# Kernel tuning notes

Hardware: AMD Instinct MI355X
Metric: run time of the kernel (lower is better)

The kernel has to match this reference:

```python
import jax, jax.numpy as jnp
import numpy as np

O_DIM, A_DIM, Z_DIM = 256, 8, 9
D, H, L, M, B = 128, 128, 4, 4, 65536  # module dim, MLP hidden, n_layers, n_modules, batch


def setup_inputs() -> dict:
    key = jax.random.key(0)
    ks = jax.random.split(key, 18)
    s = 0.05
    return {
        "o": jax.random.normal(ks[0], (B, O_DIM), jnp.float32),
        "z_map": jax.random.uniform(ks[1], (B, Z_DIM), jnp.float32),
        "collision_prob": jax.random.uniform(ks[2], (B, 1), jnp.float32),
        # base obs embedding and routing (task) embedding
        "Wb": jax.random.normal(ks[3], (O_DIM, D), jnp.float32) * s,
        "bb": jnp.zeros((D,), jnp.float32),
        "Wz": jax.random.normal(ks[4], (Z_DIM + 1, D), jnp.float32) * s,
        "bz": jnp.zeros((D,), jnp.float32),
        # L layers x M modules of DxD linears
        "Wm": jax.random.normal(ks[5], (L, M, D, D), jnp.float32) * s,
        "bm": jnp.zeros((L, M, D), jnp.float32),
        # routing heads: L-1 inter-layer (M*M) gates + final (M,) gate
        "Wg": jax.random.normal(ks[6], (L - 1, D, M * M), jnp.float32) * s,
        "Wg_last": jax.random.normal(ks[7], (D, M), jnp.float32) * s,
        # dueling heads
        "Wv": jax.random.normal(ks[8], (D, 1), jnp.float32) * s,
        "bv": jnp.zeros((1,), jnp.float32),
        "Wa1": jax.random.normal(ks[9], (D, H), jnp.float32) * s,
        "ba1": jnp.zeros((H,), jnp.float32),
        "Wa2": jax.random.normal(ks[10], (H, A_DIM), jnp.float32) * s,
        "ba2": jnp.zeros((A_DIM,), jnp.float32),
    }


def _softmodule(o, z_map, collision_prob, Wb, bb, Wz, bz, Wm, bm, Wg, Wg_last):
    f0 = jax.nn.relu(o @ Wb + bb)                              # (B, D)
    z_in = jnp.concatenate([z_map, collision_prob], axis=-1)   # (B, Z+1)
    g = jax.nn.relu(z_in @ Wz + bz) * f0                       # routing embedding (B, D)
    # layer 0: all modules consume the obs embedding
    x = jax.nn.relu(jnp.einsum("bd,mde->bme", f0, Wm[0]) + bm[0])  # (B, M, D)
    for l in range(1, L):
        logits = (g @ Wg[l - 1]).reshape(-1, M, M)             # (B, i, j)
        p = jax.nn.softmax(logits, axis=1)                     # soft routing over incoming modules i
        xin = jnp.einsum("bij,bid->bjd", p, x)                 # weighted gather-combine
        x = jax.nn.relu(jnp.einsum("bmd,mde->bme", xin, Wm[l]) + bm[l])
    p_last = jax.nn.softmax(g @ Wg_last, axis=-1)              # (B, M)
    return jnp.einsum("bm,bmd->bd", p_last, x)                 # (B, D)


def reference(o, z_map, collision_prob, Wb, bb, Wz, bz, Wm, bm, Wg, Wg_last,
              Wv, bv, Wa1, ba1, Wa2, ba2):
    feature = _softmodule(o, z_map, collision_prob, Wb, bb, Wz, bz, Wm, bm, Wg, Wg_last)
    value = feature @ Wv + bv                                  # (B, 1)
    adv = jax.nn.relu(feature @ Wa1 + ba1) @ Wa2 + ba2         # (B, A)
    adv = adv - adv.mean(axis=-1, keepdims=True)
    return adv + value
```

## Files before the change

### kernel.cpp

```cpp
#include <hip/hip_runtime.h>
#include <stdint.h>


typedef __attribute__((ext_vector_type(8))) short short8;
typedef __attribute__((ext_vector_type(4))) float f32x4;
typedef __attribute__((ext_vector_type(2))) float f32x2;
typedef __attribute__((address_space(1))) const unsigned int u32_g;
typedef __attribute__((address_space(3))) unsigned int u32_l;

__device__ __forceinline__ unsigned short f2bf(float f) {
  union { float f; uint32_t u; } v; v.f = f;
  uint32_t r = v.u + 0x7FFFu + ((v.u >> 16) & 1u);
  return (unsigned short)(r >> 16);
}
__device__ __forceinline__ float blo(uint32_t w) { union { uint32_t u; float f; } c; c.u = w << 16; return c.f; }
__device__ __forceinline__ float bhi(uint32_t w) { union { uint32_t u; float f; } c; c.u = w & 0xffff0000u; return c.f; }
__device__ __forceinline__ uint32_t packrne(float lo, float hi) {
  union { float f; uint32_t u; } a, b; a.f = lo; b.f = hi;
  uint32_t ra = a.u + 0x7fffu + ((a.u >> 16) & 1u);
  uint32_t rb = b.u + 0x7fffu + ((b.u >> 16) & 1u);
  return (ra >> 16) | (rb & 0xffff0000u);
}
__device__ __forceinline__ f32x2 unpk2(uint32_t w) {
  f32x2 r; r.x = blo(w); r.y = bhi(w); return r;
}
union S8 { short8 s; uint32_t u[4]; };

__global__ void prep_weights(const float* __restrict__ Wb, const float* __restrict__ Wm,
                             const float* __restrict__ Wa1, const float* __restrict__ Wg,
                             const float* __restrict__ Wgl, const float* __restrict__ Wa2,
                             unsigned short* __restrict__ ws) {
  int idx = blockIdx.x * 256 + threadIdx.x;
  if (idx >= 321536) return;
  unsigned short v;
  if (idx < 32768) {
    int st = idx >> 12, n = (idx >> 5) & 127, kk = idx & 31;
    v = f2bf(Wb[(st * 32 + kk) * 128 + n]);
  } else if (idx < 294912) {
    int t = idx - 32768; int lj = t >> 14; int g = t & 16383;
    int st = g >> 12, n = (g >> 5) & 127, kk = g & 31;
    v = f2bf(Wm[lj * 16384 + (st * 32 + kk) * 128 + n]);
  } else if (idx < 311296) {
    int t = idx - 294912; int st = t >> 12, n = (t >> 5) & 127, kk = t & 31;
    v = f2bf(Wa1[(st * 32 + kk) * 128 + n]);
  } else if (idx < 319488) {
    int t = idx - 311296; int st = t >> 11, n = (t >> 5) & 63, kk = t & 31;
    int k = st * 32 + kk;
    if (n < 48)      v = f2bf(Wg[(n >> 4) * 2048 + k * 16 + (n & 15)]);
    else if (n < 52) v = f2bf(Wgl[k * 4 + (n - 48)]);
    else             v = 0;
  } else {
    int t = idx - 319488; int st = t >> 9, n = (t >> 5) & 15, kk = t & 31;
    v = (n < 8) ? f2bf(Wa2[(st * 32 + kk) * 8 + n]) : (unsigned short)0;
  }
  ws[idx] = v;
}

__device__ __forceinline__ void gld16(const void* g, void* l) {
  __builtin_amdgcn_global_load_lds((u32_g*)g, (u32_l*)l, 16, 0, 0);
}

template <int BYTES>
__device__ __forceinline__ void stageW(void* wl, const unsigned short* __restrict__ src, int tid) {
  const char* g = (const char*)src;
  char* l = (char*)wl;
  int wvoff = (tid >> 6) << 10;
  int goff = wvoff | ((tid & 63) << 4);
#pragma unroll
  for (int it = 0; it < BYTES / 4096; ++it)
    gld16(g + it * 4096 + goff, l + it * 4096 + wvoff);
}

__device__ __forceinline__ void gemm128(const short8 xin[4], const unsigned short* WL,
                                        int q, int ml, f32x4 a[8]) {
#pragma unroll
  for (int nt = 0; nt < 8; ++nt) a[nt] = (f32x4){0.f, 0.f, 0.f, 0.f};
#pragma unroll
  for (int st = 0; st < 4; ++st) {
#pragma unroll
    for (int nt = 0; nt < 8; ++nt) {
      short8 bf = *(const short8*)(WL + (st * 128 + nt * 16 + ml) * 32 + q * 8);
      a[nt] = __builtin_amdgcn_mfma_f32_16x16x32_bf16(xin[st], bf, a[nt], 0, 0, 0);
    }
  }
}

__device__ __forceinline__ void combine_layer(const short8 xo[4][4],
                                              const unsigned short* __restrict__ prow,
                                              short8 xin[4][4]) {
  float p[4][4];
#pragma unroll
  for (int j = 0; j < 4; ++j) {
    uint32_t pw0 = *(const uint32_t*)(prow + j * 4);
    uint32_t pw1 = *(const uint32_t*)(prow + j * 4 + 2);
    p[j][0] = blo(pw0); p[j][1] = bhi(pw0); p[j][2] = blo(pw1); p[j][3] = bhi(pw1);
  }
#pragma unroll
  for (int st = 0; st < 4; ++st) {
    S8 x0, x1, x2, x3;
    x0.s = xo[0][st]; x1.s = xo[1][st]; x2.s = xo[2][st]; x3.s = xo[3][st];
    S8 r0, r1, r2, r3;
#pragma unroll
    for (int w = 0; w < 4; ++w) {
      f32x2 u0 = unpk2(x0.u[w]), u1 = unpk2(x1.u[w]), u2 = unpk2(x2.u[w]), u3 = unpk2(x3.u[w]);
      f32x2 s0 = p[0][0] * u0 + p[0][1] * u1 + p[0][2] * u2 + p[0][3] * u3;
      f32x2 s1 = p[1][0] * u0 + p[1][1] * u1 + p[1][2] * u2 + p[1][3] * u3;
      f32x2 s2 = p[2][0] * u0 + p[2][1] * u1 + p[2][2] * u2 + p[2][3] * u3;
      f32x2 s3 = p[3][0] * u0 + p[3][1] * u1 + p[3][2] * u2 + p[3][3] * u3;
      r0.u[w] = packrne(s0.x, s0.y); r1.u[w] = packrne(s1.x, s1.y);
      r2.u[w] = packrne(s2.x, s2.y); r3.u[w] = packrne(s3.x, s3.y);
    }
    xin[0][st] = r0.s; xin[1][st] = r1.s; xin[2][st] = r2.s; xin[3][st] = r3.s;
  }
}

__global__ __attribute__((amdgpu_flat_work_group_size(256, 256), amdgpu_waves_per_eu(2, 2)))
void dueling_fused(
    const float* __restrict__ o, const float* __restrict__ zmap, const float* __restrict__ coll,
    const float* __restrict__ bb, const float* __restrict__ Wz, const float* __restrict__ bz,
    const float* __restrict__ bm, const float* __restrict__ Wv, const float* __restrict__ bv,
    const float* __restrict__ ba1, const float* __restrict__ ba2,
    const unsigned short* __restrict__ WbF, const unsigned short* __restrict__ WmF,
    const unsigned short* __restrict__ Wa1F, const unsigned short* __restrict__ WgF,
    const unsigned short* __restrict__ Wa2F, float* __restrict__ out)
{
  __shared__ __align__(16) unsigned char smem[57344];
  unsigned short* WL    = (unsigned short*)(smem);
  float*          WLf   = (float*)(smem);
  unsigned short* xbuf  = (unsigned short*)(smem + 32768);
  unsigned short* pall  = (unsigned short*)(smem + 50176);
  float*          zbufF = (float*)(smem + 50176);
  float*          WvF   = (float*)(smem + 50176);
  float*          plast = (float*)(smem + 56320);
  float*          vbuf  = (float*)(smem + 56320);

  const int tid = threadIdx.x;
  const int wv  = tid >> 6;
  const int lane = tid & 63;
  const int q   = lane >> 4;
  const int ml  = lane & 15;
  const int row0 = blockIdx.x * 64;
  unsigned short* xbw = xbuf + wv * 2176;

  for (int i = tid; i < 640; i += 256) {
    if (i < 576) { int r = i / 9, c = i - r * 9; zbufF[r * 12 + c] = zmap[(row0 + r) * 9 + c]; }
    else         { int r = i - 576; zbufF[r * 12 + 9] = coll[row0 + r]; }
  }

  const f32x4 z4 = {0.f, 0.f, 0.f, 0.f};

  f32x4 acc[8];
#pragma unroll
  for (int nt = 0; nt < 8; ++nt) acc[nt] = z4;
  const float* orow = o + (size_t)(row0 + wv * 16 + ml) * 256;
#pragma unroll
  for (int kh = 0; kh < 2; ++kh) {
    float4 ov[8];
#pragma unroll
    for (int st = 0; st < 4; ++st) {
      const float* src = orow + kh * 128 + st * 32 + q * 8;
      ov[st * 2]     = *(const float4*)(src);
      ov[st * 2 + 1] = *(const float4*)(src + 4);
    }
    if (kh) __syncthreads();
    stageW<32768>(WL, WbF + kh * 16384, tid);
    __syncthreads();
#pragma unroll
    for (int st = 0; st < 4; ++st) {
      S8 af;
      af.u[0] = packrne(ov[st*2].x, ov[st*2].y);     af.u[1] = packrne(ov[st*2].z, ov[st*2].w);
      af.u[2] = packrne(ov[st*2+1].x, ov[st*2+1].y); af.u[3] = packrne(ov[st*2+1].z, ov[st*2+1].w);
#pragma unroll
      for (int nt = 0; nt < 8; ++nt) {
        short8 bf = *(const short8*)(WL + (st * 128 + nt * 16 + ml) * 32 + q * 8);
        acc[nt] = __builtin_amdgcn_mfma_f32_16x16x32_bf16(af.s, bf, acc[nt], 0, 0, 0);
      }
    }
  }
#pragma unroll
  for (int nt = 0; nt < 8; ++nt) {
    float bbv = bb[nt * 16 + ml];
#pragma unroll
    for (int r2 = 0; r2 < 4; ++r2) {
      float v = fmaxf(acc[nt][r2] + bbv, 0.f);
      acc[nt][r2] = v;
      xbw[(q * 4 + r2) * 136 + nt * 16 + ml] = f2bf(v);
    }
  }
  __syncthreads();
  short8 f0f[4];
#pragma unroll
  for (int st = 0; st < 4; ++st) f0f[st] = *(const short8*)(xbw + ml * 136 + st * 32 + q * 8);
  for (int i = tid; i < 1280; i += 256) WLf[i] = Wz[i];
  __syncthreads();
#pragma unroll
  for (int nt = 0; nt < 8; ++nt) {
    int col = nt * 16 + ml;
    float bzv = bz[col];
#pragma unroll
    for (int r2 = 0; r2 < 4; ++r2) {
      int row = wv * 16 + q * 4 + r2;
      float zd = bzv;
#pragma unroll
      for (int k = 0; k < 10; ++k) zd += zbufF[row * 12 + k] * WLf[k * 128 + col];
      xbw[(q * 4 + r2) * 136 + col] = f2bf(fmaxf(zd, 0.f) * acc[nt][r2]);
    }
  }
  __syncthreads();
  short8 gf[4];
#pragma unroll
  for (int st = 0; st < 4; ++st) gf[st] = *(const short8*)(xbw + ml * 136 + st * 32 + q * 8);
  stageW<16384>(WL, WgF, tid);
  __syncthreads();
#pragma unroll
  for (int nt = 0; nt < 4; ++nt) acc[nt] = z4;
#pragma unroll
  for (int st = 0; st < 4; ++st) {
#pragma unroll
    for (int nt = 0; nt < 4; ++nt) {
      short8 bf = *(const short8*)(WL + (st * 64 + nt * 16 + ml) * 32 + q * 8);
      acc[nt] = __builtin_amdgcn_mfma_f32_16x16x32_bf16(gf[st], bf, acc[nt], 0, 0, 0);
    }
  }
#pragma unroll
  for (int li = 0; li < 3; ++li) {
#pragma unroll
    for (int r2 = 0; r2 < 4; ++r2) {
      float a = acc[li][r2];
      float m = fmaxf(a, __shfl_xor(a, 4)); m = fmaxf(m, __shfl_xor(m, 8));
      float e = __expf(a - m);
      float s = e; s += __shfl_xor(s, 4); s += __shfl_xor(s, 8);
      pall[(li * 64 + wv * 16 + q * 4 + r2) * 16 + (ml & 3) * 4 + (ml >> 2)] = f2bf(e / s);
    }
  }
#pragma unroll
  for (int r2 = 0; r2 < 4; ++r2) {
    float a = acc[3][r2];
    float m = fmaxf(a, __shfl_xor(a, 1)); m = fmaxf(m, __shfl_xor(m, 2));
    float e = __expf(a - m);
    float s = e; s += __shfl_xor(s, 1); s += __shfl_xor(s, 2);
    if (ml < 4) plast[(wv * 16 + q * 4 + r2) * 4 + ml] = e / s;
  }

  short8 xo[4][4];
  f32x4 a[8];
#pragma unroll
  for (int j = 0; j < 4; ++j) {
    if (j > 0) {
#pragma unroll
      for (int st = 0; st < 4; ++st) xo[j - 1][st] = *(const short8*)(xbw + ml * 136 + st * 32 + q * 8);
    }
    __syncthreads();
    stageW<32768>(WL, WmF + j * 16384, tid);
    __syncthreads();
    gemm128(f0f, WL, q, ml, a);
#pragma unroll
    for (int nt = 0; nt < 8; ++nt) {
      float bmv = bm[j * 128 + nt * 16 + ml];
#pragma unroll
      for (int r2 = 0; r2 < 4; ++r2)
        xbw[(q * 4 + r2) * 136 + nt * 16 + ml] = f2bf(fmaxf(a[nt][r2] + bmv, 0.f));
    }
  }

  short8 xin[4][4];
  for (int l = 1; l <= 2; ++l) {
#pragma unroll
    for (int st = 0; st < 4; ++st) xo[3][st] = *(const short8*)(xbw + ml * 136 + st * 32 + q * 8);
    combine_layer(xo, pall + ((l - 1) * 64 + wv * 16 + ml) * 16, xin);
#pragma unroll
    for (int j = 0; j < 4; ++j) {
      if (j > 0) {
#pragma unroll
        for (int st = 0; st < 4; ++st) xo[j - 1][st] = *(const short8*)(xbw + ml * 136 + st * 32 + q * 8);
      }
      __syncthreads();
      stageW<32768>(WL, WmF + (l * 4 + j) * 16384, tid);
      __syncthreads();
      gemm128(xin[j], WL, q, ml, a);
#pragma unroll
      for (int nt = 0; nt < 8; ++nt) {
        float bmv = bm[(l * 4 + j) * 128 + nt * 16 + ml];
#pragma unroll
        for (int r2 = 0; r2 < 4; ++r2)
          xbw[(q * 4 + r2) * 136 + nt * 16 + ml] = f2bf(fmaxf(a[nt][r2] + bmv, 0.f));
      }
    }
  }

  f32x4 feat[8];
  {
#pragma unroll
    for (int st = 0; st < 4; ++st) xo[3][st] = *(const short8*)(xbw + ml * 136 + st * 32 + q * 8);
    combine_layer(xo, pall + (2 * 64 + wv * 16 + ml) * 16, xin);
#pragma unroll
    for (int nt = 0; nt < 8; ++nt) feat[nt] = z4;
#pragma unroll
    for (int j = 0; j < 4; ++j) {
      __syncthreads();
      stageW<32768>(WL, WmF + (12 + j) * 16384, tid);
      __syncthreads();
      gemm128(xin[j], WL, q, ml, a);
      float pl[4];
#pragma unroll
      for (int r2 = 0; r2 < 4; ++r2) pl[r2] = plast[(wv * 16 + q * 4 + r2) * 4 + j];
#pragma unroll
      for (int nt = 0; nt < 8; ++nt) {
        float bmv = bm[(12 + j) * 128 + nt * 16 + ml];
#pragma unroll
        for (int r2 = 0; r2 < 4; ++r2)
          feat[nt][r2] += pl[r2] * fmaxf(a[nt][r2] + bmv, 0.f);
      }
    }
  }

  __syncthreads();
  if (tid < 128) WvF[tid] = Wv[tid];
  if (tid == 128) WvF[128] = bv[0];
  stageW<32768>(WL, Wa1F, tid);
#pragma unroll
  for (int nt = 0; nt < 8; ++nt)
#pragma unroll
    for (int r2 = 0; r2 < 4; ++r2)
      xbw[(q * 4 + r2) * 136 + nt * 16 + ml] = f2bf(feat[nt][r2]);
  __syncthreads();
#pragma unroll
  for (int r2 = 0; r2 < 4; ++r2) {
    float v = 0.f;
#pragma unroll
    for (int nt = 0; nt < 8; ++nt) v += feat[nt][r2] * WvF[nt * 16 + ml];
    v += __shfl_xor(v, 1); v += __shfl_xor(v, 2); v += __shfl_xor(v, 4); v += __shfl_xor(v, 8);
    if (ml == 0) vbuf[wv * 16 + q * 4 + r2] = v + WvF[128];
  }
  short8 ff[4];
#pragma unroll
  for (int st = 0; st < 4; ++st) ff[st] = *(const short8*)(xbw + ml * 136 + st * 32 + q * 8);
  gemm128(ff, WL, q, ml, a);
#pragma unroll
  for (int nt = 0; nt < 8; ++nt) {
    float b1v = ba1[nt * 16 + ml];
#pragma unroll
    for (int r2 = 0; r2 < 4; ++r2)
      xbw[(q * 4 + r2) * 136 + nt * 16 + ml] = f2bf(fmaxf(a[nt][r2] + b1v, 0.f));
  }
  __syncthreads();
  stageW<4096>(WL, Wa2F, tid);
  __syncthreads();
  short8 a1f[4];
#pragma unroll
  for (int st = 0; st < 4; ++st) a1f[st] = *(const short8*)(xbw + ml * 136 + st * 32 + q * 8);
  f32x4 av = z4;
#pragma unroll
  for (int st = 0; st < 4; ++st) {
    short8 bf = *(const short8*)(WL + (st * 16 + ml) * 32 + q * 8);
    av = __builtin_amdgcn_mfma_f32_16x16x32_bf16(a1f[st], bf, av, 0, 0, 0);
  }
  float ba2v = ba2[ml & 7];
#pragma unroll
  for (int r2 = 0; r2 < 4; ++r2) {
    float aa = av[r2] + ba2v;
    float s = aa + __shfl_xor(aa, 1); s += __shfl_xor(s, 2); s += __shfl_xor(s, 4);
    if (ml < 8)
      out[(size_t)(row0 + wv * 16 + q * 4 + r2) * 8 + ml] = aa - s * 0.125f + vbuf[wv * 16 + q * 4 + r2];
  }
}

extern "C" void kernel_launch(void* const* d_in, const int* in_sizes, int n_in,
                              void* d_out, int out_size, void* d_ws, size_t ws_size,
                              hipStream_t stream) {
  const float* o   = (const float*)d_in[0];
  const float* zm  = (const float*)d_in[1];
  const float* cp  = (const float*)d_in[2];
  const float* Wb  = (const float*)d_in[3];
  const float* bb  = (const float*)d_in[4];
  const float* Wz  = (const float*)d_in[5];
  const float* bz  = (const float*)d_in[6];
  const float* Wm  = (const float*)d_in[7];
  const float* bm  = (const float*)d_in[8];
  const float* Wg  = (const float*)d_in[9];
  const float* Wgl = (const float*)d_in[10];
  const float* Wv  = (const float*)d_in[11];
  const float* bv  = (const float*)d_in[12];
  const float* Wa1 = (const float*)d_in[13];
  const float* ba1 = (const float*)d_in[14];
  const float* Wa2 = (const float*)d_in[15];
  const float* ba2 = (const float*)d_in[16];
  unsigned short* wsT = (unsigned short*)d_ws;

  int B = in_sizes[0] / 256;

  hipLaunchKernelGGL(prep_weights, dim3(1256), dim3(256), 0, stream,
                     Wb, Wm, Wa1, Wg, Wgl, Wa2, wsT);
  hipLaunchKernelGGL(dueling_fused, dim3(B / 64), dim3(256), 0, stream,
                     o, zm, cp, bb, Wz, bz, bm, Wv, bv, ba1, ba2,
                     wsT, wsT + 32768, wsT + 294912, wsT + 311296, wsT + 319488,
                     (float*)d_out);
}
```

Baseline: 251.9 us.

## Stream all weights through a triple-buffered LDS ring with async prefetch

```diff
diff --git a/kernel.cpp b/kernel.cpp
--- a/kernel.cpp
+++ b/kernel.cpp
@@ -15,6 +15,7 @@
 }
 __device__ __forceinline__ float blo(uint32_t w) { union { uint32_t u; float f; } c; c.u = w << 16; return c.f; }
 __device__ __forceinline__ float bhi(uint32_t w) { union { uint32_t u; float f; } c; c.u = w & 0xffff0000u; return c.f; }
+__device__ __forceinline__ float b2f(unsigned short h) { union { uint32_t u; float f; } c; c.u = ((uint32_t)h) << 16; return c.f; }
 __device__ __forceinline__ uint32_t packrne(float lo, float hi) {
   union { float f; uint32_t u; } a, b; a.f = lo; b.f = hi;
   uint32_t ra = a.u + 0x7fffu + ((a.u >> 16) & 1u);
@@ -36,19 +37,19 @@
   if (idx < 32768) {
     int st = idx >> 12, n = (idx >> 5) & 127, kk = idx & 31;
     v = f2bf(Wb[(st * 32 + kk) * 128 + n]);
-  } else if (idx < 294912) {
-    int t = idx - 32768; int lj = t >> 14; int g = t & 16383;
-    int st = g >> 12, n = (g >> 5) & 127, kk = g & 31;
-    v = f2bf(Wm[lj * 16384 + (st * 32 + kk) * 128 + n]);
-  } else if (idx < 311296) {
-    int t = idx - 294912; int st = t >> 12, n = (t >> 5) & 127, kk = t & 31;
-    v = f2bf(Wa1[(st * 32 + kk) * 128 + n]);
-  } else if (idx < 319488) {
-    int t = idx - 311296; int st = t >> 11, n = (t >> 5) & 63, kk = t & 31;
+  } else if (idx < 40960) {
+    int t = idx - 32768; int st = t >> 11, n = (t >> 5) & 63, kk = t & 31;
     int k = st * 32 + kk;
     if (n < 48)      v = f2bf(Wg[(n >> 4) * 2048 + k * 16 + (n & 15)]);
     else if (n < 52) v = f2bf(Wgl[k * 4 + (n - 48)]);
     else             v = 0;
+  } else if (idx < 303104) {
+    int t = idx - 40960; int lj = t >> 14; int g = t & 16383;
+    int st = g >> 12, n = (g >> 5) & 127, kk = g & 31;
+    v = f2bf(Wm[lj * 16384 + (st * 32 + kk) * 128 + n]);
+  } else if (idx < 319488) {
+    int t = idx - 303104; int st = t >> 12, n = (t >> 5) & 127, kk = t & 31;
+    v = f2bf(Wa1[(st * 32 + kk) * 128 + n]);
   } else {
     int t = idx - 319488; int st = t >> 9, n = (t >> 5) & 15, kk = t & 31;
     v = (n < 8) ? f2bf(Wa2[(st * 32 + kk) * 8 + n]) : (unsigned short)0;
@@ -60,28 +61,12 @@
   __builtin_amdgcn_global_load_lds((u32_g*)g, (u32_l*)l, 16, 0, 0);
 }
 
-template <int BYTES>
-__device__ __forceinline__ void stageW(void* wl, const unsigned short* __restrict__ src, int tid) {
-  const char* g = (const char*)src;
-  char* l = (char*)wl;
-  int wvoff = (tid >> 6) << 10;
-  int goff = wvoff | ((tid & 63) << 4);
-#pragma unroll
-  for (int it = 0; it < BYTES / 4096; ++it)
-    gld16(g + it * 4096 + goff, l + it * 4096 + wvoff);
-}
-
-__device__ __forceinline__ void gemm128(const short8 xin[4], const unsigned short* WL,
-                                        int q, int ml, f32x4 a[8]) {
-#pragma unroll
-  for (int nt = 0; nt < 8; ++nt) a[nt] = (f32x4){0.f, 0.f, 0.f, 0.f};
-#pragma unroll
-  for (int st = 0; st < 4; ++st) {
-#pragma unroll
-    for (int nt = 0; nt < 8; ++nt) {
-      short8 bf = *(const short8*)(WL + (st * 128 + nt * 16 + ml) * 32 + q * 8);
-      a[nt] = __builtin_amdgcn_mfma_f32_16x16x32_bf16(xin[st], bf, a[nt], 0, 0, 0);
-    }
+__device__ __forceinline__ void gemm32(const short8 xst, const unsigned short* C,
+                                       int q, int ml, f32x4 a[8]) {
+#pragma unroll
+  for (int nt = 0; nt < 8; ++nt) {
+    short8 bf = *(const short8*)(C + (nt * 16 + ml) * 32 + q * 8);
+    a[nt] = __builtin_amdgcn_mfma_f32_16x16x32_bf16(xst, bf, a[nt], 0, 0, 0);
   }
 }
 
@@ -114,25 +99,26 @@
   }
 }
 
-__global__ __attribute__((amdgpu_flat_work_group_size(256, 256), amdgpu_waves_per_eu(2, 2)))
+#define RSYNC2() asm volatile("s_waitcnt vmcnt(2) lgkmcnt(0)\n\ts_barrier" ::: "memory")
+#define RSYNC0() asm volatile("s_waitcnt vmcnt(0) lgkmcnt(0)\n\ts_barrier" ::: "memory")
+#define RSTEP2(PTR) do { RSYNC2(); ring_issue(); (PTR) = ring_next(); } while (0)
+#define RSTEP0(PTR) do { RSYNC0(); ring_issue(); (PTR) = ring_next(); } while (0)
+
+__global__ __attribute__((amdgpu_flat_work_group_size(256, 256), amdgpu_waves_per_eu(3)))
 void dueling_fused(
     const float* __restrict__ o, const float* __restrict__ zmap, const float* __restrict__ coll,
     const float* __restrict__ bb, const float* __restrict__ Wz, const float* __restrict__ bz,
     const float* __restrict__ bm, const float* __restrict__ Wv, const float* __restrict__ bv,
     const float* __restrict__ ba1, const float* __restrict__ ba2,
-    const unsigned short* __restrict__ WbF, const unsigned short* __restrict__ WmF,
-    const unsigned short* __restrict__ Wa1F, const unsigned short* __restrict__ WgF,
-    const unsigned short* __restrict__ Wa2F, float* __restrict__ out)
+    const unsigned short* __restrict__ ws, float* __restrict__ out)
 {
-  __shared__ __align__(16) unsigned char smem[57344];
-  unsigned short* WL    = (unsigned short*)(smem);
-  float*          WLf   = (float*)(smem);
-  unsigned short* xbuf  = (unsigned short*)(smem + 32768);
-  unsigned short* pall  = (unsigned short*)(smem + 50176);
-  float*          zbufF = (float*)(smem + 50176);
-  float*          WvF   = (float*)(smem + 50176);
-  float*          plast = (float*)(smem + 56320);
-  float*          vbuf  = (float*)(smem + 56320);
+  __shared__ __align__(16) unsigned char smem[53248];
+  unsigned short* xbuf  = (unsigned short*)(smem + 24576);
+  unsigned short* pall  = (unsigned short*)(smem + 41984);
+  float*          zbufF = (float*)(smem + 41984);
+  float*          plast = (float*)(smem + 48128);
+  float*          vbuf  = (float*)(smem + 48128);
+  unsigned short* bmL   = (unsigned short*)(smem + 49152);
 
   const int tid = threadIdx.x;
   const int wv  = tid >> 6;
@@ -146,37 +132,51 @@
     if (i < 576) { int r = i / 9, c = i - r * 9; zbufF[r * 12 + c] = zmap[(row0 + r) * 9 + c]; }
     else         { int r = i - 576; zbufF[r * 12 + 9] = coll[row0 + r]; }
   }
+  for (int i = tid; i < 2048; i += 256) bmL[i] = f2bf(bm[i]);
+
+  short8 of[8];
+  const float* orow = o + (size_t)(row0 + wv * 16 + ml) * 256;
+#pragma unroll
+  for (int st = 0; st < 8; ++st) {
+    float4 v0 = *(const float4*)(orow + st * 32 + q * 8);
+    float4 v1 = *(const float4*)(orow + st * 32 + q * 8 + 4);
+    S8 af;
+    af.u[0] = packrne(v0.x, v0.y); af.u[1] = packrne(v0.z, v0.w);
+    af.u[2] = packrne(v1.x, v1.y); af.u[3] = packrne(v1.z, v1.w);
+    of[st] = af.s;
+  }
+  asm volatile("s_waitcnt vmcnt(0) lgkmcnt(0)" ::: "memory");
+
+  int r_kiss = 0, r_riss = 0, r_rc = 0;
+  const char* r_gsrc = (const char*)ws;
+  const int wvoff = wv << 10;
+  const int goff  = wvoff | ((tid & 63) << 4);
+  auto ring_issue = [&]() {
+    if (r_kiss <= 78) {
+      char* l = (char*)smem + r_riss;
+      int srco = (r_kiss == 78) ? 0 : 4096;
+      gld16(r_gsrc + goff, l + wvoff);
+      gld16(r_gsrc + srco + goff, l + 4096 + wvoff);
+      r_gsrc += 8192;
+    }
+    ++r_kiss;
+    r_riss += 8192; if (r_riss == 24576) r_riss = 0;
+  };
+  auto ring_next = [&]() -> const unsigned short* {
+    const unsigned short* p = (const unsigned short*)(smem + r_rc);
+    r_rc += 8192; if (r_rc == 24576) r_rc = 0;
+    return p;
+  };
+  ring_issue(); ring_issue();
 
   const f32x4 z4 = {0.f, 0.f, 0.f, 0.f};
+  const unsigned short* C;
 
   f32x4 acc[8];
 #pragma unroll
   for (int nt = 0; nt < 8; ++nt) acc[nt] = z4;
-  const float* orow = o + (size_t)(row0 + wv * 16 + ml) * 256;
-#pragma unroll
-  for (int kh = 0; kh < 2; ++kh) {
-    float4 ov[8];
-#pragma unroll
-    for (int st = 0; st < 4; ++st) {
-      const float* src = orow + kh * 128 + st * 32 + q * 8;
-      ov[st * 2]     = *(const float4*)(src);
-      ov[st * 2 + 1] = *(const float4*)(src + 4);
-    }
-    if (kh) __syncthreads();
-    stageW<32768>(WL, WbF + kh * 16384, tid);
-    __syncthreads();
-#pragma unroll
-    for (int st = 0; st < 4; ++st) {
-      S8 af;
-      af.u[0] = packrne(ov[st*2].x, ov[st*2].y);     af.u[1] = packrne(ov[st*2].z, ov[st*2].w);
-      af.u[2] = packrne(ov[st*2+1].x, ov[st*2+1].y); af.u[3] = packrne(ov[st*2+1].z, ov[st*2+1].w);
-#pragma unroll
-      for (int nt = 0; nt < 8; ++nt) {
-        short8 bf = *(const short8*)(WL + (st * 128 + nt * 16 + ml) * 32 + q * 8);
-        acc[nt] = __builtin_amdgcn_mfma_f32_16x16x32_bf16(af.s, bf, acc[nt], 0, 0, 0);
-      }
-    }
-  }
+#pragma unroll
+  for (int st = 0; st < 8; ++st) { RSTEP2(C); gemm32(of[st], C, q, ml, acc); }
 #pragma unroll
   for (int nt = 0; nt < 8; ++nt) {
     float bbv = bb[nt * 16 + ml];
@@ -187,41 +187,48 @@
       xbw[(q * 4 + r2) * 136 + nt * 16 + ml] = f2bf(v);
     }
   }
-  __syncthreads();
   short8 f0f[4];
 #pragma unroll
   for (int st = 0; st < 4; ++st) f0f[st] = *(const short8*)(xbw + ml * 136 + st * 32 + q * 8);
-  for (int i = tid; i < 1280; i += 256) WLf[i] = Wz[i];
-  __syncthreads();
+
 #pragma unroll
   for (int nt = 0; nt < 8; ++nt) {
     int col = nt * 16 + ml;
+    float wz[10];
+#pragma unroll
+    for (int k = 0; k < 10; ++k) wz[k] = Wz[k * 128 + col];
     float bzv = bz[col];
 #pragma unroll
     for (int r2 = 0; r2 < 4; ++r2) {
       int row = wv * 16 + q * 4 + r2;
       float zd = bzv;
 #pragma unroll
-      for (int k = 0; k < 10; ++k) zd += zbufF[row * 12 + k] * WLf[k * 128 + col];
+      for (int k = 0; k < 10; ++k) zd += zbufF[row * 12 + k] * wz[k];
       xbw[(q * 4 + r2) * 136 + col] = f2bf(fmaxf(zd, 0.f) * acc[nt][r2]);
     }
   }
-  __syncthreads();
   short8 gf[4];
 #pragma unroll
   for (int st = 0; st < 4; ++st) gf[st] = *(const short8*)(xbw + ml * 136 + st * 32 + q * 8);
-  stageW<16384>(WL, WgF, tid);
-  __syncthreads();
+
 #pragma unroll
   for (int nt = 0; nt < 4; ++nt) acc[nt] = z4;
-#pragma unroll
-  for (int st = 0; st < 4; ++st) {
+  RSTEP0(C);
+#pragma unroll
+  for (int sp = 0; sp < 2; ++sp)
 #pragma unroll
     for (int nt = 0; nt < 4; ++nt) {
-      short8 bf = *(const short8*)(WL + (st * 64 + nt * 16 + ml) * 32 + q * 8);
-      acc[nt] = __builtin_amdgcn_mfma_f32_16x16x32_bf16(gf[st], bf, acc[nt], 0, 0, 0);
-    }
-  }
+      short8 bf = *(const short8*)(C + (sp * 64 + nt * 16 + ml) * 32 + q * 8);
+      acc[nt] = __builtin_amdgcn_mfma_f32_16x16x32_bf16(gf[sp], bf, acc[nt], 0, 0, 0);
+    }
+  RSTEP2(C);
+#pragma unroll
+  for (int sp = 0; sp < 2; ++sp)
+#pragma unroll
+    for (int nt = 0; nt < 4; ++nt) {
+      short8 bf = *(const short8*)(C + (sp * 64 + nt * 16 + ml) * 32 + q * 8);
+      acc[nt] = __builtin_amdgcn_mfma_f32_16x16x32_bf16(gf[2 + sp], bf, acc[nt], 0, 0, 0);
+    }
 #pragma unroll
   for (int li = 0; li < 3; ++li) {
 #pragma unroll
@@ -250,13 +257,13 @@
 #pragma unroll
       for (int st = 0; st < 4; ++st) xo[j - 1][st] = *(const short8*)(xbw + ml * 136 + st * 32 + q * 8);
     }
-    __syncthreads();
-    stageW<32768>(WL, WmF + j * 16384, tid);
-    __syncthreads();
-    gemm128(f0f, WL, q, ml, a);
+#pragma unroll
+    for (int nt = 0; nt < 8; ++nt) a[nt] = z4;
+#pragma unroll
+    for (int st = 0; st < 4; ++st) { RSTEP2(C); gemm32(f0f[st], C, q, ml, a); }
 #pragma unroll
     for (int nt = 0; nt < 8; ++nt) {
-      float bmv = bm[j * 128 + nt * 16 + ml];
+      float bmv = b2f(bmL[j * 128 + nt * 16 + ml]);
 #pragma unroll
       for (int r2 = 0; r2 < 4; ++r2)
         xbw[(q * 4 + r2) * 136 + nt * 16 + ml] = f2bf(fmaxf(a[nt][r2] + bmv, 0.f));
@@ -274,13 +281,13 @@
 #pragma unroll
         for (int st = 0; st < 4; ++st) xo[j - 1][st] = *(const short8*)(xbw + ml * 136 + st * 32 + q * 8);
       }
-      __syncthreads();
-      stageW<32768>(WL, WmF + (l * 4 + j) * 16384, tid);
-      __syncthreads();
-      gemm128(xin[j], WL, q, ml, a);
+#pragma unroll
+      for (int nt = 0; nt < 8; ++nt) a[nt] = z4;
+#pragma unroll
+      for (int st = 0; st < 4; ++st) { RSTEP2(C); gemm32(xin[j][st], C, q, ml, a); }
 #pragma unroll
       for (int nt = 0; nt < 8; ++nt) {
-        float bmv = bm[(l * 4 + j) * 128 + nt * 16 + ml];
+        float bmv = b2f(bmL[(l * 4 + j) * 128 + nt * 16 + ml]);
 #pragma unroll
         for (int r2 = 0; r2 < 4; ++r2)
           xbw[(q * 4 + r2) * 136 + nt * 16 + ml] = f2bf(fmaxf(a[nt][r2] + bmv, 0.f));
@@ -297,16 +304,16 @@
     for (int nt = 0; nt < 8; ++nt) feat[nt] = z4;
 #pragma unroll
     for (int j = 0; j < 4; ++j) {
-      __syncthreads();
-      stageW<32768>(WL, WmF + (12 + j) * 16384, tid);
-      __syncthreads();
-      gemm128(xin[j], WL, q, ml, a);
+#pragma unroll
+      for (int nt = 0; nt < 8; ++nt) a[nt] = z4;
+#pragma unroll
+      for (int st = 0; st < 4; ++st) { RSTEP2(C); gemm32(xin[j][st], C, q, ml, a); }
       float pl[4];
 #pragma unroll
       for (int r2 = 0; r2 < 4; ++r2) pl[r2] = plast[(wv * 16 + q * 4 + r2) * 4 + j];
 #pragma unroll
       for (int nt = 0; nt < 8; ++nt) {
-        float bmv = bm[(12 + j) * 128 + nt * 16 + ml];
+        float bmv = b2f(bmL[(12 + j) * 128 + nt * 16 + ml]);
 #pragma unroll
         for (int r2 = 0; r2 < 4; ++r2)
           feat[nt][r2] += pl[r2] * fmaxf(a[nt][r2] + bmv, 0.f);
@@ -314,28 +321,34 @@
     }
   }
 
-  __syncthreads();
-  if (tid < 128) WvF[tid] = Wv[tid];
-  if (tid == 128) WvF[128] = bv[0];
-  stageW<32768>(WL, Wa1F, tid);
 #pragma unroll
   for (int nt = 0; nt < 8; ++nt)
 #pragma unroll
     for (int r2 = 0; r2 < 4; ++r2)
       xbw[(q * 4 + r2) * 136 + nt * 16 + ml] = f2bf(feat[nt][r2]);
-  __syncthreads();
-#pragma unroll
-  for (int r2 = 0; r2 < 4; ++r2) {
-    float v = 0.f;
-#pragma unroll
-    for (int nt = 0; nt < 8; ++nt) v += feat[nt][r2] * WvF[nt * 16 + ml];
-    v += __shfl_xor(v, 1); v += __shfl_xor(v, 2); v += __shfl_xor(v, 4); v += __shfl_xor(v, 8);
-    if (ml == 0) vbuf[wv * 16 + q * 4 + r2] = v + WvF[128];
-  }
   short8 ff[4];
 #pragma unroll
   for (int st = 0; st < 4; ++st) ff[st] = *(const short8*)(xbw + ml * 136 + st * 32 + q * 8);
-  gemm128(ff, WL, q, ml, a);
+#pragma unroll
+  for (int nt = 0; nt < 8; ++nt) a[nt] = z4;
+#pragma unroll
+  for (int st = 0; st < 4; ++st) { RSTEP2(C); gemm32(ff[st], C, q, ml, a); }
+
+  {
+    float wvv[8];
+#pragma unroll
+    for (int nt = 0; nt < 8; ++nt) wvv[nt] = Wv[nt * 16 + ml];
+    float bvv = bv[0];
+#pragma unroll
+    for (int r2 = 0; r2 < 4; ++r2) {
+      float v = 0.f;
+#pragma unroll
+      for (int nt = 0; nt < 8; ++nt) v += feat[nt][r2] * wvv[nt];
+      v += __shfl_xor(v, 1); v += __shfl_xor(v, 2); v += __shfl_xor(v, 4); v += __shfl_xor(v, 8);
+      if (ml == 0) vbuf[wv * 16 + q * 4 + r2] = v + bvv;
+    }
+  }
+
 #pragma unroll
   for (int nt = 0; nt < 8; ++nt) {
     float b1v = ba1[nt * 16 + ml];
@@ -343,16 +356,15 @@
     for (int r2 = 0; r2 < 4; ++r2)
       xbw[(q * 4 + r2) * 136 + nt * 16 + ml] = f2bf(fmaxf(a[nt][r2] + b1v, 0.f));
   }
-  __syncthreads();
-  stageW<4096>(WL, Wa2F, tid);
-  __syncthreads();
   short8 a1f[4];
 #pragma unroll
   for (int st = 0; st < 4; ++st) a1f[st] = *(const short8*)(xbw + ml * 136 + st * 32 + q * 8);
+
+  RSTEP0(C);
   f32x4 av = z4;
 #pragma unroll
   for (int st = 0; st < 4; ++st) {
-    short8 bf = *(const short8*)(WL + (st * 16 + ml) * 32 + q * 8);
+    short8 bf = *(const short8*)(C + (st * 16 + ml) * 32 + q * 8);
     av = __builtin_amdgcn_mfma_f32_16x16x32_bf16(a1f[st], bf, av, 0, 0, 0);
   }
   float ba2v = ba2[ml & 7];
@@ -393,6 +405,5 @@
                      Wb, Wm, Wa1, Wg, Wgl, Wa2, wsT);
   hipLaunchKernelGGL(dueling_fused, dim3(B / 64), dim3(256), 0, stream,
                      o, zm, cp, bb, Wz, bz, bm, Wv, bv, ba1, ba2,
-                     wsT, wsT + 32768, wsT + 294912, wsT + 311296, wsT + 319488,
-                     (float*)d_out);
-}
+                     wsT, (float*)d_out);
+}
```

Measured after the change: 239.2 us. 1.05x faster.
